# Optimization experiments

Measured on AMD Instinct MI355X. Metric: run time of the kernel, lower is better.

The kernel has to match this reference:

```python
import jax, jax.numpy as jnp
import numpy as np

H = 4            # attention heads
C = 128          # hidden_size (per-head channels; concat=False -> mean over heads)
ET = 5           # edge types
IN = 512         # input feature dim
NCLS = 153
N_TOTAL = 100000
N_SRC = (40000, 20000)
N_DST = (30000, 10000)
BATCH = (25000, 8000)
E = (200000, 80000)
EPS = 1e-5


def bn(x, g, b):
    # BatchNorm1d, training-mode batch statistics (biased var), affine
    mu = x.mean(0)
    var = x.var(0)
    return (x - mu) / jnp.sqrt(var + EPS) * g + b


def gat(x_src, src, dst, n_dst, W, att_s, att_d, bias):
    # PyG GATConv, bipartite (x_src, x_src[:n_dst]), shared lin, concat=False
    x = (x_src @ W).reshape(-1, H, C)            # [Ns, H, C]
    a_s = (x * att_s).sum(-1)                    # [Ns, H]
    a_d = (x[:n_dst] * att_d).sum(-1)            # [Nd, H]
    logits = jax.nn.leaky_relu(a_s[src] + a_d[dst], 0.2)   # [E, H]
    m = jax.ops.segment_max(logits, dst, num_segments=n_dst)
    e = jnp.exp(logits - m[dst])
    s = jax.ops.segment_sum(e, dst, num_segments=n_dst)
    coef = e / jnp.maximum(s[dst], 1e-16)        # segment softmax over in-edges
    out = jax.ops.segment_sum(coef[:, :, None] * x[src], dst, num_segments=n_dst)
    return out.mean(1) + bias                    # [Nd, C]


def _layer(feature, li, nodes_idx, src, dst, Ws, bs, bng, bnb, Wg, attS, attD, bg, wp, bp, pg, pb):
    batch, n_dst = BATCH[li], N_DST[li]
    skip = jax.nn.elu(bn(feature @ Ws + bs, bng[0], bnb[0]))
    feats = [skip[:batch]]
    for e2 in range(ET):  # small fixed set of structurally distinct edge types
        xs = feature[nodes_idx[e2]]
        o = gat(xs, src[e2], dst[e2], n_dst, Wg[e2], attS[e2], attD[e2], bg[e2])
        feats.append(jax.nn.elu(bn(o, bng[e2 + 1], bnb[e2 + 1]))[:batch])
    temp = jnp.stack(feats, 1)                   # [batch, ET+1, C]
    attn = jax.nn.softmax(temp @ wp + bp, axis=1)  # [batch, ET+1, 1]
    sk = jnp.einsum('bp,bpc->bc', attn[..., 0], temp)
    return bn(sk, pg, pb)                        # dropout is identity at inference


def setup_inputs():
    key = jax.random.key(0)
    keys = iter(jax.random.split(key, 48))
    def nrm(shape, scale):
        return jax.random.normal(next(keys), shape, dtype=jnp.float32) * scale
    def ri(shape, hi):
        return jax.random.randint(next(keys), shape, 0, hi, dtype=jnp.int32)
    inp = {}
    inp['feature'] = nrm((N_TOTAL, IN), 1.0)
    inp['nodes_idx0'] = ri((ET, N_SRC[0]), N_TOTAL)
    inp['edge_src0'] = ri((ET, E[0]), N_SRC[0])
    inp['edge_dst0'] = jnp.sort(ri((ET, E[0]), N_DST[0]), axis=-1)
    inp['nodes_idx1'] = ri((ET, N_SRC[1]), BATCH[0])
    inp['edge_src1'] = ri((ET, E[1]), N_SRC[1])
    inp['edge_dst1'] = jnp.sort(ri((ET, E[1]), N_DST[1]), axis=-1)
    for l, din in ((0, IN), (1, C)):
        s = str(l)
        sc = 1.0 / float(np.sqrt(din))
        inp['W_skip' + s] = nrm((din, C), sc)
        inp['b_skip' + s] = jnp.zeros((C,), jnp.float32)
        inp['bn_g' + s] = jnp.ones((ET + 1, C), jnp.float32)
        inp['bn_b' + s] = jnp.zeros((ET + 1, C), jnp.float32)
        inp['Wg' + s] = nrm((ET, din, H * C), sc)
        inp['attS' + s] = nrm((ET, H, C), 0.1)
        inp['attD' + s] = nrm((ET, H, C), 0.1)
        inp['bg' + s] = jnp.zeros((ET, C), jnp.float32)
        inp['wp' + s] = nrm((C, 1), 1.0 / float(np.sqrt(C)))
        inp['bp' + s] = jnp.zeros((1,), jnp.float32)
        inp['pg' + s] = jnp.ones((C,), jnp.float32)
        inp['pb' + s] = jnp.zeros((C,), jnp.float32)
    inp['Wm1'] = nrm((C, C), 1.0 / float(np.sqrt(C)))
    inp['bm1'] = jnp.zeros((C,), jnp.float32)
    inp['mg'] = jnp.ones((C,), jnp.float32)
    inp['mb'] = jnp.zeros((C,), jnp.float32)
    inp['Wm2'] = nrm((C, NCLS), 1.0 / float(np.sqrt(C)))
    inp['bm2'] = jnp.zeros((NCLS,), jnp.float32)
    return inp


def reference(feature, nodes_idx0, edge_src0, edge_dst0, nodes_idx1, edge_src1, edge_dst1,
              W_skip0, b_skip0, bn_g0, bn_b0, Wg0, attS0, attD0, bg0, wp0, bp0, pg0, pb0,
              W_skip1, b_skip1, bn_g1, bn_b1, Wg1, attS1, attD1, bg1, wp1, bp1, pg1, pb1,
              Wm1, bm1, mg, mb, Wm2, bm2):
    f = _layer(feature, 0, nodes_idx0, edge_src0, edge_dst0,
               W_skip0, b_skip0, bn_g0, bn_b0, Wg0, attS0, attD0, bg0, wp0, bp0, pg0, pb0)
    f = _layer(f, 1, nodes_idx1, edge_src1, edge_dst1,
               W_skip1, b_skip1, bn_g1, bn_b1, Wg1, attS1, attD1, bg1, wp1, bp1, pg1, pb1)
    h = jax.nn.relu(bn(f @ Wm1 + bm1, mg, mb))
    return h @ Wm2 + bm2
```

## Files before the change

### kernel.cpp

```cpp
#include <hip/hip_runtime.h>
#include <math.h>

#define EPSV 1e-5f
#define NSTATB 960

typedef __attribute__((ext_vector_type(8))) short short8;
typedef __attribute__((ext_vector_type(4))) float floatx4;
typedef _Float16 half2v __attribute__((ext_vector_type(2)));

__device__ __forceinline__ float waveSum(float v) {
#pragma unroll
  for (int off = 32; off > 0; off >>= 1) v += __shfl_xor(v, off, 64);
  return v;
}

__device__ __forceinline__ unsigned bfr(float f) {
  union { float f; unsigned u; } v;
  v.f = f;
  return (v.u + 0x7FFFu + ((v.u >> 16) & 1u)) >> 16;
}

__device__ __forceinline__ void gload16(const short* g, short* l) {
  __builtin_amdgcn_global_load_lds(
      (const __attribute__((address_space(1))) void*)g,
      (__attribute__((address_space(3))) void*)l, 16, 0, 0);
}

__global__ __launch_bounds__(256) void conv_bf16(const float* __restrict__ x,
                                                 short* __restrict__ y, long n4) {
  long i = (long)blockIdx.x * 256 + threadIdx.x;
  long stride = (long)gridDim.x * 256;
  for (; i < n4; i += stride) {
    float4 v = reinterpret_cast<const float4*>(x)[i];
    short4 o;
    o.x = (short)bfr(v.x);
    o.y = (short)bfr(v.y);
    o.z = (short)bfr(v.z);
    o.w = (short)bfr(v.w);
    reinterpret_cast<short4*>(y)[i] = o;
  }
}

__global__ __launch_bounds__(256) void wT_bf16(const float* __restrict__ W0,
                                               short* __restrict__ Wt0, int K, int N,
                                               long wz) {
  const float* W = W0 + (size_t)blockIdx.z * wz;
  short* Wt = Wt0 + (size_t)blockIdx.z * wz;
  __shared__ short t[32][33];
  int k0 = blockIdx.x * 32, n0 = blockIdx.y * 32;
  int x = threadIdx.x & 31, y = threadIdx.x >> 5;
#pragma unroll
  for (int dy = 0; dy < 32; dy += 8) {
    int k = k0 + y + dy, n = n0 + x;
    t[y + dy][x] = (k < K && n < N) ? (short)bfr(W[(size_t)k * N + n]) : (short)0;
  }
  __syncthreads();
#pragma unroll
  for (int dy = 0; dy < 32; dy += 8) {
    int n = n0 + y + dy, k = k0 + x;
    if (n < N && k < K) Wt[(size_t)n * K + k] = t[x][y + dy];
  }
}

#define ASZ (256 * 32)
#define BSZ (128 * 32)
__global__ __launch_bounds__(512, 4) void gemm_mfma(
    const short* __restrict__ A, const short* __restrict__ Wt0,
    const float* __restrict__ bias, float* __restrict__ Y0,
    _Float16* __restrict__ Yh0, const int* __restrict__ idx0,
    int M, int K, int N, int mTiles, int nTiles,
    long wtZ, long yZ, int idxZ,
    const float* __restrict__ attS0, const float* __restrict__ attD0,
    float* __restrict__ a_s0, float* __restrict__ a_d0, int n_dst) {
  __shared__ short Alds[3 * ASZ];
  __shared__ short Blds[3 * BSZ];
  __shared__ float sred[256][2];
  int z = blockIdx.z;
  int mt, nt;
  if (nTiles == 1) {
    mt = blockIdx.x;
    nt = 0;
  } else {
    int id = blockIdx.x;
    int slot = id >> 3;
    nt = slot & 3;
    mt = ((slot >> 2) << 3) + (id & 7);
  }
  if (mt >= mTiles) return;
  const short* Wt = Wt0 + (size_t)z * wtZ;
  const int* idx = idx0 ? (idx0 + (size_t)z * idxZ) : nullptr;
  int tid = threadIdx.x;
  int m0 = mt * 256, n0 = nt * 128;

  int srow = tid >> 2, sc = tid & 3;
  int rA0 = srow, rA1 = 128 + srow;
  int swzA0 = sc ^ ((rA0 >> 1) & 3);
  int swzA1 = sc ^ ((rA1 >> 1) & 3);
  int swzB = swzA0;
  int gr0 = m0 + rA0, gr1 = m0 + rA1;
  int ar0 = (gr0 < M) ? (idx ? idx[gr0] : gr0) : 0;
  int ar1 = (gr1 < M) ? (idx ? idx[gr1] : gr1) : 0;
  const short* aSrc0 = A + (size_t)ar0 * K + swzA0 * 8;
  const short* aSrc1 = A + (size_t)ar1 * K + swzA1 * 8;
  const short* bSrc = Wt + (size_t)(n0 + srow) * K + swzB * 8;
  int wv = tid >> 6, lane = tid & 63;
  int dA0 = wv * 512;
  int dA1 = 4096 + wv * 512;
  int dB = wv * 512;

  int wm = (wv & 3) * 64, wn = (wv >> 2) * 64;
  int lr = lane & 15, quad = lane >> 4;
  int aoff[4], boff[4];
#pragma unroll
  for (int i = 0; i < 4; i++) {
    int R = wm + i * 16 + lr;
    aoff[i] = R * 32 + ((quad ^ ((R >> 1) & 3)) << 3);
  }
#pragma unroll
  for (int j = 0; j < 4; j++) {
    int R = wn + j * 16 + lr;
    boff[j] = R * 32 + ((quad ^ ((R >> 1) & 3)) << 3);
  }

  floatx4 acc[4][4];
#pragma unroll
  for (int i = 0; i < 4; i++)
#pragma unroll
    for (int j = 0; j < 4; j++) acc[i][j] = (floatx4)0.f;

  auto stage = [&](int slot, int k) {
    gload16(aSrc0 + k, &Alds[slot * ASZ + dA0]);
    gload16(aSrc1 + k, &Alds[slot * ASZ + dA1]);
    gload16(bSrc + k, &Blds[slot * BSZ + dB]);
  };
  auto compute = [&](int slot) {
    const short* Ab = &Alds[slot * ASZ];
    const short* Bb = &Blds[slot * BSZ];
    short8 af[4], bfv[4];
#pragma unroll
    for (int i = 0; i < 4; i++)
      af[i] = *reinterpret_cast<const short8*>(&Ab[aoff[i]]);
#pragma unroll
    for (int j = 0; j < 4; j++)
      bfv[j] = *reinterpret_cast<const short8*>(&Bb[boff[j]]);
#pragma unroll
    for (int i = 0; i < 4; i++)
#pragma unroll
      for (int j = 0; j < 4; j++)
        acc[i][j] = __builtin_amdgcn_mfma_f32_16x16x32_bf16(af[i], bfv[j],
                                                            acc[i][j], 0, 0, 0);
  };

  stage(0, 0);
  stage(1, 32);
  int NT = K >> 5;
  int cur = 0, nxt = 2;
  for (int t = 0; t < NT; ++t) {
    if (t + 1 < NT) {
      asm volatile("s_waitcnt vmcnt(3)" : : : "memory");
    } else {
      asm volatile("s_waitcnt vmcnt(0)" : : : "memory");
    }
    __builtin_amdgcn_s_barrier();
    __builtin_amdgcn_sched_barrier(0);
    if (t + 2 < NT) stage(nxt, 32 * (t + 2));
    compute(cur);
    cur = (cur == 2) ? 0 : cur + 1;
    nxt = (nxt == 2) ? 0 : nxt + 1;
  }

#pragma unroll
  for (int i = 0; i < 4; i++) {
#pragma unroll
    for (int j = 0; j < 4; j++) {
      int n = n0 + wn + j * 16 + lr;
      float bv = bias ? bias[n] : 0.f;
#pragma unroll
      for (int r = 0; r < 4; r++) {
        int m = m0 + wm + i * 16 + quad * 4 + r;
        if (m < M) {
          float v = acc[i][j][r] + bv;
          if (Yh0) {
            _Float16* Yh = Yh0 + (size_t)z * yZ;
            Yh[(size_t)m * N + n] = (_Float16)v;
          } else {
            float* Y = Y0 + (size_t)z * yZ;
            Y[(size_t)m * N + n] = v;
          }
        }
      }
    }
  }
  if (attS0) {
    int h = nt;
    const float* aSb = attS0 + z * 512 + h * 128;
    const float* aDb = attD0 + z * 512 + h * 128;
    float* asv = a_s0 + (size_t)z * M * 4;
    float* adv = a_d0 + (size_t)z * n_dst * 4;
#pragma unroll
    for (int p = 0; p < 2; p++) {
      const float* av = p ? aDb : aSb;
      float w[4];
#pragma unroll
      for (int j = 0; j < 4; j++) w[j] = av[wn + j * 16 + lr];
#pragma unroll
      for (int i = 0; i < 4; i++) {
#pragma unroll
        for (int r = 0; r < 4; r++) {
          float v = acc[i][0][r] * w[0] + acc[i][1][r] * w[1] +
                    acc[i][2][r] * w[2] + acc[i][3][r] * w[3];
          v += __shfl_xor(v, 1, 64);
          v += __shfl_xor(v, 2, 64);
          v += __shfl_xor(v, 4, 64);
          v += __shfl_xor(v, 8, 64);
          if (lr == 0) sred[wm + i * 16 + quad * 4 + r][wv >> 2] = v;
        }
      }
      __syncthreads();
      if (tid < 256) {
        int m = m0 + tid;
        if (m < M) {
          float s = sred[tid][0] + sred[tid][1];
          if (p == 0) asv[(size_t)m * 4 + h] = s;
          else if (m < n_dst) adv[(size_t)m * 4 + h] = s;
        }
      }
      __syncthreads();
    }
  }
}

__global__ __launch_bounds__(256) void gemm_bias(
    const float* __restrict__ A, const float* __restrict__ W,
    const float* __restrict__ bias, float* __restrict__ Y,
    const int* __restrict__ idx, int M, int K, int N) {
  __shared__ float As[16][65];
  __shared__ float Bs[16][64];
  int tid = threadIdx.x;
  int tx = tid & 15, ty = tid >> 4;
  int m0 = blockIdx.x * 64, n0 = blockIdx.y * 64;
  float acc[4][4] = {};
  for (int k0 = 0; k0 < K; k0 += 16) {
    for (int l = tid; l < 64 * 16; l += 256) {
      int r = l >> 4, kk = l & 15;
      int row = m0 + r;
      float v = 0.f;
      if (row < M) {
        int ar = idx ? idx[row] : row;
        v = A[(size_t)ar * K + k0 + kk];
      }
      As[kk][r] = v;
    }
    for (int l = tid; l < 16 * 64; l += 256) {
      int kk = l >> 6, n = l & 63;
      int col = n0 + n;
      Bs[kk][n] = (col < N) ? W[(size_t)(k0 + kk) * N + col] : 0.f;
    }
    __syncthreads();
#pragma unroll
    for (int kk = 0; kk < 16; kk++) {
      float a[4], b[4];
#pragma unroll
      for (int i = 0; i < 4; i++) a[i] = As[kk][ty + 16 * i];
#pragma unroll
      for (int j = 0; j < 4; j++) b[j] = Bs[kk][tx + 16 * j];
#pragma unroll
      for (int i = 0; i < 4; i++)
#pragma unroll
        for (int j = 0; j < 4; j++) acc[i][j] += a[i] * b[j];
    }
    __syncthreads();
  }
#pragma unroll
  for (int i = 0; i < 4; i++) {
    int m = m0 + ty + 16 * i;
    if (m >= M) continue;
#pragma unroll
    for (int j = 0; j < 4; j++) {
      int n = n0 + tx + 16 * j;
      if (n < N) Y[(size_t)m * N + n] = acc[i][j] + (bias ? bias[n] : 0.f);
    }
  }
}

__global__ void build_starts(const int* __restrict__ dst0, int E, int n_dst,
                             int* __restrict__ starts0) {
  const int* dst = dst0 + (size_t)blockIdx.y * E;
  int* starts = starts0 + (size_t)blockIdx.y * (n_dst + 1);
  int k = blockIdx.x * 256 + threadIdx.x;
  if (k > E) return;
  if (k == 0) {
    int d0 = dst[0];
    for (int j = 0; j <= d0; j++) starts[j] = 0;
  } else if (k < E) {
    int d = dst[k], dp = dst[k - 1];
    for (int j = dp + 1; j <= d; j++) starts[j] = k;
  } else {
    int dl = dst[E - 1];
    for (int j = dl + 1; j <= n_dst; j++) starts[j] = E;
  }
}

__global__ void edge_logits(const int* __restrict__ src0, const int* __restrict__ dst0,
                            const float* __restrict__ a_s0, const float* __restrict__ a_d0,
                            float* __restrict__ logits0, int E, int asZ, int adZ) {
  int z = blockIdx.y;
  const int* src = src0 + (size_t)z * E;
  const int* dst = dst0 + (size_t)z * E;
  const float* a_s = a_s0 + (size_t)z * asZ;
  const float* a_d = a_d0 + (size_t)z * adZ;
  float* logits = logits0 + (size_t)z * E * 4;
  int k = blockIdx.x * 256 + threadIdx.x;
  if (k >= E) return;
  int s = src[k], d = dst[k];
#pragma unroll
  for (int h = 0; h < 4; h++) {
    float v = a_s[s * 4 + h] + a_d[d * 4 + h];
    v = (v >= 0.f) ? v : 0.2f * v;
    logits[k * 4 + h] = v;
  }
}

__global__ void node_ms(const float* __restrict__ logits0, const int* __restrict__ starts0,
                        float* __restrict__ ms0, int n_dst, int E) {
  int z = blockIdx.y;
  const float* logits = logits0 + (size_t)z * E * 4;
  const int* starts = starts0 + (size_t)z * (n_dst + 1);
  float* ms = ms0 + (size_t)z * n_dst * 8;
  int t = blockIdx.x * 256 + threadIdx.x;
  int j = t >> 2, h = t & 3;
  if (j >= n_dst) return;
  int r0 = starts[j], r1 = starts[j + 1];
  float m = -1e30f;
  for (int k = r0; k < r1; k++) m = fmaxf(m, logits[k * 4 + h]);
  float s = 0.f;
  for (int k = r0; k < r1; k++) s += __expf(logits[k * 4 + h] - m);
  ms[j * 8 + h] = m;
  ms[j * 8 + 4 + h] = s;
}

__global__ __launch_bounds__(64) void gat_aggregate(
    const _Float16* __restrict__ x0, const float* __restrict__ lg0,
    const int* __restrict__ src0, const int* __restrict__ starts0,
    const float* __restrict__ ms0, const float* __restrict__ bg0,
    float* __restrict__ o0, int n_dst, long xZ, int E) {
  int z = blockIdx.y;
  const _Float16* x = x0 + (size_t)z * xZ;
  const float* lg = lg0 + (size_t)z * E * 4;
  const int* src = src0 + (size_t)z * E;
  const int* starts = starts0 + (size_t)z * (n_dst + 1);
  const float* ms = ms0 + (size_t)z * n_dst * 8;
  const float* bg = bg0 + z * 128;
  float* o = o0 + (size_t)z * (size_t)n_dst * 128;
  int j = blockIdx.x;
  int t = threadIdx.x;
  int r0 = starts[j], r1 = starts[j + 1];
  float m0 = ms[j * 8 + 0], m1 = ms[j * 8 + 1];
  float m2 = ms[j * 8 + 2], m3 = ms[j * 8 + 3];
  float i0 = 1.f / fmaxf(ms[j * 8 + 4], 1e-16f);
  float i1 = 1.f / fmaxf(ms[j * 8 + 5], 1e-16f);
  float i2 = 1.f / fmaxf(ms[j * 8 + 6], 1e-16f);
  float i3 = 1.f / fmaxf(ms[j * 8 + 7], 1e-16f);
  float a00 = 0.f, a01 = 0.f, a10 = 0.f, a11 = 0.f;
  float a20 = 0.f, a21 = 0.f, a30 = 0.f, a31 = 0.f;
  for (int k = r0; k < r1; k++) {
    int s = src[k];
    const half2v* xr = reinterpret_cast<const half2v*>(x + (size_t)s * 512);
    half2v v0 = xr[t];
    half2v v1 = xr[64 + t];
    half2v v2 = xr[128 + t];
    half2v v3 = xr[192 + t];
    float c0 = __expf(lg[k * 4 + 0] - m0) * i0;
    float c1 = __expf(lg[k * 4 + 1] - m1) * i1;
    float c2 = __expf(lg[k * 4 + 2] - m2) * i2;
    float c3 = __expf(lg[k * 4 + 3] - m3) * i3;
    a00 += c0 * (float)v0[0];
    a01 += c0 * (float)v0[1];
    a10 += c1 * (float)v1[0];
    a11 += c1 * (float)v1[1];
    a20 += c2 * (float)v2[0];
    a21 += c2 * (float)v2[1];
    a30 += c3 * (float)v3[0];
    a31 += c3 * (float)v3[1];
  }
  float2 out;
  out.x = 0.25f * (a00 + a10 + a20 + a30) + bg[2 * t];
  out.y = 0.25f * (a01 + a11 + a21 + a31) + bg[2 * t + 1];
  *reinterpret_cast<float2*>(&o[(size_t)j * 128 + 2 * t]) = out;
}

__global__ __launch_bounds__(128) void bn_partial(const float* __restrict__ x0, long xZ,
                                                  float* __restrict__ partial0, int N) {
  const float* x = x0 + (size_t)blockIdx.y * xZ;
  float* partial = partial0 + (size_t)blockIdx.y * (NSTATB * 256);
  int c = threadIdx.x;
  float s = 0.f, ss = 0.f;
  for (int r = blockIdx.x; r < N; r += gridDim.x) {
    float v = x[(size_t)r * 128 + c];
    s += v;
    ss += v * v;
  }
  partial[blockIdx.x * 256 + c] = s;
  partial[blockIdx.x * 256 + 128 + c] = ss;
}

__global__ __launch_bounds__(64) void bn_finalize(const float* __restrict__ partial0,
                                                  int G, int N, float* __restrict__ stats0) {
  const float* partial = partial0 + (size_t)blockIdx.y * (NSTATB * 256);
  float* stats = stats0 + blockIdx.y * 256;
  int c = blockIdx.x;
  int lane = threadIdx.x;
  float s = 0.f, ss = 0.f;
  for (int b = lane; b < G; b += 64) {
    s += partial[b * 256 + c];
    ss += partial[b * 256 + 128 + c];
  }
  s = waveSum(s);
  ss = waveSum(ss);
  if (lane == 0) {
    float mu = s / (float)N;
    float var = ss / (float)N - mu * mu;
    stats[c] = mu;
    stats[128 + c] = rsqrtf(var + EPSV);
  }
}

__global__ __launch_bounds__(128) void bn_apply(
    const float* __restrict__ x0, long xZ, const float* __restrict__ stats0,
    const float* __restrict__ g0, const float* __restrict__ b0, int gz,
    float* __restrict__ y0, short* __restrict__ yb0, long yZ, int M,
    int ostride, int act) {
  int z = blockIdx.y;
  const float* x = x0 + (size_t)z * xZ;
  const float* stats = stats0 + z * 256;
  const float* g = g0 + z * gz;
  const float* b = b0 + z * gz;
  int r = blockIdx.x;
  int c = threadIdx.x;
  if (r >= M) return;
  float v = x[(size_t)r * 128 + c];
  v = (v - stats[c]) * stats[128 + c] * g[c] + b[c];
  if (act == 1) v = (v > 0.f) ? v : (__expf(v) - 1.f);
  if (act == 2) v = fmaxf(v, 0.f);
  if (yb0) {
    short* yb = yb0 + (size_t)z * yZ;
    yb[(size_t)r * ostride + c] = (short)bfr(v);
  } else {
    float* y = y0 + (size_t)z * yZ;
    y[(size_t)r * ostride + c] = v;
  }
}

__global__ __launch_bounds__(128) void pool_attn(
    const float* __restrict__ temp, const float* __restrict__ wp,
    const float* __restrict__ bp, float* __restrict__ sk, int batch) {
  int b = blockIdx.x, c = threadIdx.x;
  int lane = c & 63, wid = c >> 6;
  __shared__ float red[12];
  const float* tr = temp + (size_t)b * 768;
  float wpc = wp[c];
  float t[6];
#pragma unroll
  for (int p = 0; p < 6; p++) t[p] = tr[p * 128 + c];
#pragma unroll
  for (int p = 0; p < 6; p++) {
    float v = waveSum(t[p] * wpc);
    if (lane == 0) red[wid * 6 + p] = v;
  }
  __syncthreads();
  float z[6], m = -1e30f;
#pragma unroll
  for (int p = 0; p < 6; p++) {
    z[p] = red[p] + red[6 + p] + bp[0];
    m = fmaxf(m, z[p]);
  }
  float es = 0.f;
#pragma unroll
  for (int p = 0; p < 6; p++) {
    z[p] = __expf(z[p] - m);
    es += z[p];
  }
  float inv = 1.f / es;
  float o = 0.f;
#pragma unroll
  for (int p = 0; p < 6; p++) o += z[p] * inv * t[p];
  sk[(size_t)b * 128 + c] = o;
}

extern "C" void kernel_launch(void* const* d_in, const int* in_sizes, int n_in,
                              void* d_out, int out_size, void* d_ws, size_t ws_size,
                              hipStream_t stream) {
  const float* feature = (const float*)d_in[0];
  const int* nodes_idx[2] = {(const int*)d_in[1], (const int*)d_in[4]};
  const int* edge_src[2] = {(const int*)d_in[2], (const int*)d_in[5]};
  const int* edge_dst[2] = {(const int*)d_in[3], (const int*)d_in[6]};
  const float *Wsk[2], *bsk[2], *bng[2], *bnb[2], *Wg[2], *attS[2], *attD[2],
      *bg[2], *wp[2], *bp[2], *pg[2], *pb[2];
  for (int l = 0; l < 2; l++) {
    int base = 7 + l * 12;
    Wsk[l] = (const float*)d_in[base + 0];
    bsk[l] = (const float*)d_in[base + 1];
    bng[l] = (const float*)d_in[base + 2];
    bnb[l] = (const float*)d_in[base + 3];
    Wg[l] = (const float*)d_in[base + 4];
    attS[l] = (const float*)d_in[base + 5];
    attD[l] = (const float*)d_in[base + 6];
    bg[l] = (const float*)d_in[base + 7];
    wp[l] = (const float*)d_in[base + 8];
    bp[l] = (const float*)d_in[base + 9];
    pg[l] = (const float*)d_in[base + 10];
    pb[l] = (const float*)d_in[base + 11];
  }
  const float* Wm1 = (const float*)d_in[31];
  const float* bm1 = (const float*)d_in[32];
  const float* mg = (const float*)d_in[33];
  const float* mb = (const float*)d_in[34];
  const float* Wm2 = (const float*)d_in[35];
  const float* bm2 = (const float*)d_in[36];

  float* ws = (float*)d_ws;
  float* bufG5 = ws;   ws += 102400000;
  float* bufSkip = ws; ws += 12800000;
  float* bufO5 = ws;   ws += 19200000;
  float* temp = ws;    ws += 19200000;
  float* f1 = ws;      ws += 1024000;
  float* bufH = ws;    ws += 1024000;
  float* a_s5 = ws;    ws += 800000;
  float* a_d5 = ws;    ws += 600000;
  float* logi5 = ws;   ws += 4000000;
  float* ms5 = ws;     ws += 1200000;
  float* part = ws;    ws += 5 * NSTATB * 256;
  float* stats = ws;   ws += 5 * 256;
  int* starts5a = (int*)ws; ws += 150080;
  int* starts5b = (int*)ws; ws += 50080;
  short* featB = (short*)ws; ws += 25600000;
  short* f0b = (short*)ws;   ws += 1600000;
  short* wt_sk0 = (short*)ws; ws += 32768;
  short* wt_g0 = (short*)ws;  ws += 655360;
  short* wt_sk1 = (short*)ws; ws += 8192;
  short* wt_g1 = (short*)ws;  ws += 163840;
  _Float16* bufG5h = (_Float16*)bufG5;

  auto cdiv = [](int a, int b) { return (a + b - 1) / b; };

  build_starts<<<dim3(cdiv(200001, 256), 5), 256, 0, stream>>>(edge_dst[0],
                                                               200000, 30000, starts5a);
  build_starts<<<dim3(cdiv(80001, 256), 5), 256, 0, stream>>>(edge_dst[1],
                                                              80000, 10000, starts5b);
  conv_bf16<<<2048, 256, 0, stream>>>(feature, featB, 100000L * 512 / 4);
  wT_bf16<<<dim3(16, 4, 1), 256, 0, stream>>>(Wsk[0], wt_sk0, 512, 128, 0);
  wT_bf16<<<dim3(16, 16, 5), 256, 0, stream>>>(Wg[0], wt_g0, 512, 512, 512L * 512);
  wT_bf16<<<dim3(4, 4, 1), 256, 0, stream>>>(Wsk[1], wt_sk1, 128, 128, 0);
  wT_bf16<<<dim3(4, 16, 5), 256, 0, stream>>>(Wg[1], wt_g1, 128, 512, 512L * 128);

  auto run_layer = [&](const short* Xb, int Nf, int din, int li, float* fout,
                       short* foutb, const short* wt_sk, const short* wt_g,
                       int* starts5) {
    const int Nsrc = (li == 0) ? 40000 : 20000;
    const int n_dst = (li == 0) ? 30000 : 10000;
    const int batch = (li == 0) ? 25000 : 8000;
    const int E = (li == 0) ? 200000 : 80000;
    const int mtS = cdiv(Nf, 256);
    const int mtG = cdiv(Nsrc, 256);
    const int GpG = cdiv(mtG, 8) * 8;

    gemm_mfma<<<dim3(mtS, 1, 1), 512, 0, stream>>>(
        Xb, wt_sk, bsk[li], bufSkip, nullptr, nullptr, Nf, din, 128, mtS, 1,
        0, 0, 0, nullptr, nullptr, nullptr, nullptr, 0);
    bn_partial<<<dim3(NSTATB, 1), 128, 0, stream>>>(bufSkip, 0, part, Nf);
    bn_finalize<<<dim3(128, 1), 64, 0, stream>>>(part, NSTATB, Nf, stats);
    bn_apply<<<dim3(batch, 1), 128, 0, stream>>>(bufSkip, 0, stats, bng[li],
                                                 bnb[li], 0, temp, nullptr, 0,
                                                 batch, 768, 1);

    gemm_mfma<<<dim3(GpG * 4, 1, 5), 512, 0, stream>>>(
        Xb, wt_g, nullptr, nullptr, bufG5h, nodes_idx[li], Nsrc, din, 512,
        mtG, 4, (long)din * 512, (long)Nsrc * 512, Nsrc,
        attS[li], attD[li], a_s5, a_d5, n_dst);
    edge_logits<<<dim3(cdiv(E, 256), 5), 256, 0, stream>>>(
        edge_src[li], edge_dst[li], a_s5, a_d5, logi5, E, Nsrc * 4, n_dst * 4);
    node_ms<<<dim3(cdiv(n_dst * 4, 256), 5), 256, 0, stream>>>(logi5, starts5,
                                                               ms5, n_dst, E);
    gat_aggregate<<<dim3(n_dst, 5), 64, 0, stream>>>(
        bufG5h, logi5, edge_src[li], starts5, ms5, bg[li], bufO5, n_dst,
        (long)Nsrc * 512, E);
    bn_partial<<<dim3(NSTATB, 5), 128, 0, stream>>>(bufO5, (long)n_dst * 128,
                                                    part, n_dst);
    bn_finalize<<<dim3(128, 5), 64, 0, stream>>>(part, NSTATB, n_dst, stats);
    bn_apply<<<dim3(batch, 5), 128, 0, stream>>>(
        bufO5, (long)n_dst * 128, stats, bng[li] + 128, bnb[li] + 128, 128,
        temp + 128, nullptr, 128, batch, 768, 1);

    pool_attn<<<batch, 128, 0, stream>>>(temp, wp[li], bp[li], bufSkip, batch);
    bn_partial<<<dim3(NSTATB, 1), 128, 0, stream>>>(bufSkip, 0, part, batch);
    bn_finalize<<<dim3(128, 1), 64, 0, stream>>>(part, NSTATB, batch, stats);
    bn_apply<<<dim3(batch, 1), 128, 0, stream>>>(bufSkip, 0, stats, pg[li], pb[li],
                                                 0, fout, foutb, 0, batch, 128, 0);
  };

  run_layer(featB, 100000, 512, 0, nullptr, f0b, wt_sk0, wt_g0, starts5a);
  run_layer(f0b, 25000, 128, 1, f1, nullptr, wt_sk1, wt_g1, starts5b);

  gemm_bias<<<dim3(cdiv(8000, 64), 2), 256, 0, stream>>>(f1, Wm1, bm1, bufSkip,
                                                         nullptr, 8000, 128, 128);
  bn_partial<<<dim3(NSTATB, 1), 128, 0, stream>>>(bufSkip, 0, part, 8000);
  bn_finalize<<<dim3(128, 1), 64, 0, stream>>>(part, NSTATB, 8000, stats);
  bn_apply<<<8000, 128, 0, stream>>>(bufSkip, 0, stats, mg, mb, 0, bufH,
                                     nullptr, 0, 8000, 128, 2);
  gemm_bias<<<dim3(cdiv(8000, 64), 3), 256, 0, stream>>>(
      bufH, Wm2, bm2, (float*)d_out, nullptr, 8000, 128, 153);
}
```

Measured before the change: 1.311 ms.

## Fuse BN-apply and ELU into pooling kernel; simplify GEMM to double buffering

Removes the two bn_apply launches that wrote normalized skip and GAT outputs into the temp buffer. pool_fused now reads the raw skip and GAT outputs and applies batchnorm and ELU inline, which saves a write and re-read of the large stacked tensor. The stats buffer is enlarged so all six per-branch statistics stay live. Separately, the MFMA GEMM drops from a triple-buffered pipeline with explicit vmcnt waits to a simple double-buffered loop with __syncthreads. That frees LDS but likely exposes more load latency.

```diff
diff --git a/kernel.cpp b/kernel.cpp
--- a/kernel.cpp
+++ b/kernel.cpp
@@ -72,8 +72,8 @@
     long wtZ, long yZ, int idxZ,
     const float* __restrict__ attS0, const float* __restrict__ attD0,
     float* __restrict__ a_s0, float* __restrict__ a_d0, int n_dst) {
-  __shared__ short Alds[3 * ASZ];
-  __shared__ short Blds[3 * BSZ];
+  __shared__ short Alds[2 * ASZ];
+  __shared__ short Blds[2 * BSZ];
   __shared__ float sred[256][2];
   int z = blockIdx.z;
   int mt, nt;
@@ -152,21 +152,11 @@
   };
 
   stage(0, 0);
-  stage(1, 32);
   int NT = K >> 5;
-  int cur = 0, nxt = 2;
   for (int t = 0; t < NT; ++t) {
-    if (t + 1 < NT) {
-      asm volatile("s_waitcnt vmcnt(3)" : : : "memory");
-    } else {
-      asm volatile("s_waitcnt vmcnt(0)" : : : "memory");
-    }
-    __builtin_amdgcn_s_barrier();
-    __builtin_amdgcn_sched_barrier(0);
-    if (t + 2 < NT) stage(nxt, 32 * (t + 2));
-    compute(cur);
-    cur = (cur == 2) ? 0 : cur + 1;
-    nxt = (nxt == 2) ? 0 : nxt + 1;
+    __syncthreads();
+    if (t + 1 < NT) stage((t + 1) & 1, 32 * (t + 1));
+    compute(t & 1);
   }
 
 #pragma unroll
@@ -451,17 +441,28 @@
   }
 }
 
-__global__ __launch_bounds__(128) void pool_attn(
-    const float* __restrict__ temp, const float* __restrict__ wp,
+__global__ __launch_bounds__(128) void pool_fused(
+    const float* __restrict__ skipB, const float* __restrict__ o5, long oZ,
+    const float* __restrict__ stats, const float* __restrict__ g6,
+    const float* __restrict__ b6, const float* __restrict__ wp,
     const float* __restrict__ bp, float* __restrict__ sk, int batch) {
   int b = blockIdx.x, c = threadIdx.x;
   int lane = c & 63, wid = c >> 6;
   __shared__ float red[12];
-  const float* tr = temp + (size_t)b * 768;
   float wpc = wp[c];
   float t[6];
-#pragma unroll
-  for (int p = 0; p < 6; p++) t[p] = tr[p * 128 + c];
+  {
+    float v = skipB[(size_t)b * 128 + c];
+    v = (v - stats[c]) * stats[128 + c] * g6[c] + b6[c];
+    t[0] = (v > 0.f) ? v : (__expf(v) - 1.f);
+  }
+#pragma unroll
+  for (int p = 1; p < 6; p++) {
+    const float* st = stats + p * 256;
+    float v = o5[(size_t)(p - 1) * oZ + (size_t)b * 128 + c];
+    v = (v - st[c]) * st[128 + c] * g6[p * 128 + c] + b6[p * 128 + c];
+    t[p] = (v > 0.f) ? v : (__expf(v) - 1.f);
+  }
 #pragma unroll
   for (int p = 0; p < 6; p++) {
     float v = waveSum(t[p] * wpc);
@@ -530,7 +531,7 @@
   float* logi5 = ws;   ws += 4000000;
   float* ms5 = ws;     ws += 1200000;
   float* part = ws;    ws += 5 * NSTATB * 256;
-  float* stats = ws;   ws += 5 * 256;
+  float* stats = ws;   ws += 7 * 256;
   int* starts5a = (int*)ws; ws += 150080;
   int* starts5b = (int*)ws; ws += 50080;
   short* featB = (short*)ws; ws += 25600000;
@@ -569,9 +570,6 @@
         0, 0, 0, nullptr, nullptr, nullptr, nullptr, 0);
     bn_partial<<<dim3(NSTATB, 1), 128, 0, stream>>>(bufSkip, 0, part, Nf);
     bn_finalize<<<dim3(128, 1), 64, 0, stream>>>(part, NSTATB, Nf, stats);
-    bn_apply<<<dim3(batch, 1), 128, 0, stream>>>(bufSkip, 0, stats, bng[li],
-                                                 bnb[li], 0, temp, nullptr, 0,
-                                                 batch, 768, 1);
 
     gemm_mfma<<<dim3(GpG * 4, 1, 5), 512, 0, stream>>>(
         Xb, wt_g, nullptr, nullptr, bufG5h, nodes_idx[li], Nsrc, din, 512,
@@ -586,16 +584,18 @@
         (long)Nsrc * 512, E);
     bn_partial<<<dim3(NSTATB, 5), 128, 0, stream>>>(bufO5, (long)n_dst * 128,
                                                     part, n_dst);
-    bn_finalize<<<dim3(128, 5), 64, 0, stream>>>(part, NSTATB, n_dst, stats);
-    bn_apply<<<dim3(batch, 5), 128, 0, stream>>>(
-        bufO5, (long)n_dst * 128, stats, bng[li] + 128, bnb[li] + 128, 128,
-        temp + 128, nullptr, 128, batch, 768, 1);
-
-    pool_attn<<<batch, 128, 0, stream>>>(temp, wp[li], bp[li], bufSkip, batch);
-    bn_partial<<<dim3(NSTATB, 1), 128, 0, stream>>>(bufSkip, 0, part, batch);
-    bn_finalize<<<dim3(128, 1), 64, 0, stream>>>(part, NSTATB, batch, stats);
-    bn_apply<<<dim3(batch, 1), 128, 0, stream>>>(bufSkip, 0, stats, pg[li], pb[li],
-                                                 0, fout, foutb, 0, batch, 128, 0);
+    bn_finalize<<<dim3(128, 5), 64, 0, stream>>>(part, NSTATB, n_dst,
+                                                 stats + 256);
+
+    pool_fused<<<batch, 128, 0, stream>>>(bufSkip, bufO5, (long)n_dst * 128,
+                                          stats, bng[li], bnb[li], wp[li],
+                                          bp[li], temp, batch);
+    bn_partial<<<dim3(NSTATB, 1), 128, 0, stream>>>(temp, 0, part, batch);
+    bn_finalize<<<dim3(128, 1), 64, 0, stream>>>(part, NSTATB, batch,
+                                                 stats + 6 * 256);
+    bn_apply<<<dim3(batch, 1), 128, 0, stream>>>(temp, 0, stats + 6 * 256,
+                                                 pg[li], pb[li], 0, fout, foutb,
+                                                 0, batch, 128, 0);
   };
 
   run_layer(featB, 100000, 512, 0, nullptr, f0b, wt_sk0, wt_g0, starts5a);
@@ -605,8 +605,8 @@
                                                          nullptr, 8000, 128, 128);
   bn_partial<<<dim3(NSTATB, 1), 128, 0, stream>>>(bufSkip, 0, part, 8000);
   bn_finalize<<<dim3(128, 1), 64, 0, stream>>>(part, NSTATB, 8000, stats);
-  bn_apply<<<8000, 128, 0, stream>>>(bufSkip, 0, stats, mg, mb, 0, bufH,
-                                     nullptr, 0, 8000, 128, 2);
+  bn_apply<<<dim3(8000, 1), 128, 0, stream>>>(bufSkip, 0, stats, mg, mb, 0,
+                                              bufH, nullptr, 0, 8000, 128, 2);
   gemm_bias<<<dim3(cdiv(8000, 64), 3), 256, 0, stream>>>(
       bufH, Wm2, bm2, (float*)d_out, nullptr, 8000, 128, 153);
 }
```

Result: faster. 1.243 ms (-5.2%).
